# Kernel optimization log

Measured on AMD Instinct MI355X. Metric: run time of the kernel, lower is better.

Reference implementation:

```python
import jax, jax.numpy as jnp
from jax import lax
import numpy as np

# dims
B, C, H, W, T = 8, 2, 64, 64, 200
# per-layer neuron configs (defaults from NetworkBasic.__init__)
THETA = (30.0, 50.0, 100.0)
TAU_SR = (1.0, 2.0, 4.0)
TAU_REF = (1.0, 2.0, 4.0)
SCALE_REF = (1.0, 1.0, 1.0)
TAU_RHO = (1.0, 1.0, 10.0)


def psp(x, tau):
    """SLAYER synaptic response: first-order leaky integration over time axis (last).
    a[t] = exp(-1/tau) * a[t-1] + x[t]"""
    d = jnp.exp(jnp.asarray(-1.0 / tau, x.dtype))
    xt = jnp.moveaxis(x, -1, 0)  # [T, B, C, H, W]
    def step(a, xi):
        a = d * a + xi
        return a, a
    _, ys = lax.scan(step, jnp.zeros_like(xt[0]), xt)
    return jnp.moveaxis(ys, 0, -1)


def spike(u, theta, tau_ref, scale_ref, tau_rho):
    """SLAYER spiking unit: threshold + leaky refractory state, sequential over T.
    Forward emits hard spikes; surrogate (sigmoid) used only for gradients."""
    dref = jnp.exp(jnp.asarray(-1.0 / tau_ref, u.dtype))
    th = jnp.asarray(theta, u.dtype)
    ut = jnp.moveaxis(u, -1, 0)  # [T, ...]
    def step(r, ui):
        v = ui + r
        hard = (v >= th).astype(u.dtype)
        sur = jax.nn.sigmoid((v - th) / tau_rho)
        s = sur + lax.stop_gradient(hard - sur)  # straight-through surrogate
        r2 = dref * r - th * scale_ref * s       # refractory subtraction
        return r2, s
    _, s = lax.scan(step, jnp.zeros_like(ut[0]), ut)
    return jnp.moveaxis(s, 0, -1)


def conv2d_t(x, w, pad):
    """slayer.conv: spatial conv applied independently per timestep (kernel kxkx1, no bias)."""
    Bb, Cc, Hh, Ww, Tt = x.shape
    xt = jnp.moveaxis(x, -1, 1).reshape(Bb * Tt, Cc, Hh, Ww)
    y = lax.conv_general_dilated(xt, w, (1, 1), [(pad, pad), (pad, pad)],
                                 dimension_numbers=("NCHW", "OIHW", "NCHW"))
    O = w.shape[0]
    return jnp.moveaxis(y.reshape(Bb, Tt, O, Hh, Ww), 1, -1)


def convT2d_t(x, w):
    """slayer.convTranspose kernel=2 stride=2, per timestep (exact 2x upsample)."""
    Bb, Cc, Hh, Ww, Tt = x.shape
    xt = jnp.moveaxis(x, -1, 1).reshape(Bb * Tt, Cc, Hh, Ww)
    y = lax.conv_transpose(xt, w, (2, 2), "VALID",
                           dimension_numbers=("NCHW", "OIHW", "NCHW"))
    O = w.shape[0]
    return jnp.moveaxis(y.reshape(Bb, Tt, O, 2 * Hh, 2 * Ww), 1, -1)


def setup_inputs() -> dict:
    key = jax.random.key(0)
    k0, k1, k2, k3 = jax.random.split(key, 4)
    spikeInput = (jax.random.uniform(k0, (B, C, H, W, T)) < 0.3).astype(jnp.float32)
    w1 = jax.random.normal(k1, (8, 2, 5, 5), jnp.float32) * 10.0
    w2 = jax.random.normal(k2, (8, 8, 3, 3), jnp.float32) * 10.0
    wup = jax.random.normal(k3, (2, 8, 2, 2), jnp.float32) * 10.0
    return {"spikeInput": spikeInput, "w1": w1, "w2": w2, "wup": wup}


def reference(spikeInput, w1, w2, wup):
    Bb, Cc, Hh, Ww, Tt = spikeInput.shape
    psp1 = psp(spikeInput, TAU_SR[0])
    psp1_up = jax.image.resize(psp1, (Bb, Cc, 2 * Hh, 2 * Ww, Tt), method="linear")
    s1 = spike(conv2d_t(psp1, w1, 2), THETA[0], TAU_REF[0], SCALE_REF[0], TAU_RHO[0])
    s2 = spike(conv2d_t(psp(s1, TAU_SR[1]), w2, 1), THETA[1], TAU_REF[1], SCALE_REF[1], TAU_RHO[1])
    s3 = spike(convT2d_t(psp(s2, TAU_SR[2]), wup) + psp1_up,
               THETA[2], TAU_REF[2], SCALE_REF[2], TAU_RHO[2])
    return s3
```

## Files before the change

kernel.cpp:

```cpp
#include <hip/hip_runtime.h>

#define DEC1 0.36787944117144233f
#define DEC2 0.60653065971263342f
#define DEC3 0.77880078307140487f

__global__ void prep_weights(const float* __restrict__ w1,
                             const float* __restrict__ w2,
                             const float* __restrict__ wup,
                             float* __restrict__ wr)
{
    int i = blockIdx.x * 256 + threadIdx.x;
    if (i < 400) {
        int o = i & 7, tap = i >> 3;
        int c = tap / 25, rem = tap % 25, ky = rem / 5, kx = rem % 5;
        wr[i] = w1[((o * 2 + c) * 5 + ky) * 5 + kx];
    }
    if (i < 576) {
        int o = i & 7, tap = i >> 3;
        int c = tap / 9, rem = tap % 9, ky = rem / 3, kx = rem % 3;
        wr[400 + i] = w2[((o * 8 + c) * 3 + ky) * 3 + kx];
    }
    if (i < 64) {
        int c = i & 7, r = i >> 3;
        int dj = r & 1, di = (r >> 1) & 1, o = r >> 2;
        wr[976 + i] = wup[((o * 8 + c) * 2 + (1 - di)) * 2 + (1 - dj)];
    }
}

static __device__ __forceinline__ float4 spike_psp4(float4 u, float th, float dref,
                                                    float dq, float& r, float& q)
{
    float4 qv; float v, s;
    v = __fadd_rn(u.x, r); s = (v >= th) ? 1.f : 0.f;
    r = __fsub_rn(__fmul_rn(dref, r), __fmul_rn(th, s));
    q = __fadd_rn(__fmul_rn(dq, q), s); qv.x = q;
    v = __fadd_rn(u.y, r); s = (v >= th) ? 1.f : 0.f;
    r = __fsub_rn(__fmul_rn(dref, r), __fmul_rn(th, s));
    q = __fadd_rn(__fmul_rn(dq, q), s); qv.y = q;
    v = __fadd_rn(u.z, r); s = (v >= th) ? 1.f : 0.f;
    r = __fsub_rn(__fmul_rn(dref, r), __fmul_rn(th, s));
    q = __fadd_rn(__fmul_rn(dq, q), s); qv.z = q;
    v = __fadd_rn(u.w, r); s = (v >= th) ? 1.f : 0.f;
    r = __fsub_rn(__fmul_rn(dref, r), __fmul_rn(th, s));
    q = __fadd_rn(__fmul_rn(dq, q), s); qv.w = q;
    return qv;
}

static __device__ __forceinline__ float4 spike4(float4 u, float th, float dref, float& r)
{
    float4 ov; float v, s;
    v = __fadd_rn(u.x, r); s = (v >= th) ? 1.f : 0.f;
    r = __fsub_rn(__fmul_rn(dref, r), __fmul_rn(th, s)); ov.x = s;
    v = __fadd_rn(u.y, r); s = (v >= th) ? 1.f : 0.f;
    r = __fsub_rn(__fmul_rn(dref, r), __fmul_rn(th, s)); ov.y = s;
    v = __fadd_rn(u.z, r); s = (v >= th) ? 1.f : 0.f;
    r = __fsub_rn(__fmul_rn(dref, r), __fmul_rn(th, s)); ov.z = s;
    v = __fadd_rn(u.w, r); s = (v >= th) ? 1.f : 0.f;
    r = __fsub_rn(__fmul_rn(dref, r), __fmul_rn(th, s)); ov.w = s;
    return ov;
}

#define FMA4(ACC_, W_, D_) { ACC_.x += (W_)*(D_).x; ACC_.y += (W_)*(D_).y; \
                             ACC_.z += (W_)*(D_).z; ACC_.w += (W_)*(D_).w; }

#define PSP4(V_, X_, st) { \
    V_.x = __fadd_rn(__fmul_rn(DEC1, st),   X_.x); \
    V_.y = __fadd_rn(__fmul_rn(DEC1, V_.x), X_.y); \
    V_.z = __fadd_rn(__fmul_rn(DEC1, V_.y), X_.z); \
    V_.w = __fadd_rn(__fmul_rn(DEC1, V_.z), X_.w); st = V_.w; }

__global__ __launch_bounds__(256, 2)
void snn_fused(const float* __restrict__ spk,
               const float* __restrict__ wr,
               float* __restrict__ out)
{
    const int tid  = threadIdx.x;
    const int b    = blockIdx.x >> 6;
    const int tile = blockIdx.x & 63;
    const int gy0  = (tile >> 3) << 3;
    const int gx0  = (tile & 7) << 3;

    __shared__ float4 sP1[2][2][2][224];
    __shared__ float4 sP2[8][2][100];
    __shared__ float4 sP3[8][2][64];

    float aP0 = 0.f, aP1 = 0.f;
    float rB[4], qB[4];
    float rC[2] = {0.f, 0.f}, qC[2] = {0.f, 0.f};
    float r3[2] = {0.f, 0.f};
#pragma unroll
    for (int i = 0; i < 4; ++i) { rB[i] = 0.f; qB[i] = 0.f; }

    const int ary = tid / 14, arx = tid % 14;
    const int aidx = ary * 16 + arx;
    const int aiy = gy0 - 3 + ary, aix = gx0 - 3 + arx;
    const bool avalid = (tid < 196) && (aiy >= 0) && (aiy < 64) && (aix >= 0) && (aix < 64);
    const int aoff0 = avalid ? (((b * 2 + 0) * 64 + aiy) * 64 + aix) * 200 : 0;
    const int aoff1 = avalid ? (((b * 2 + 1) * 64 + aiy) * 64 + aix) * 200 : 0;

    const int ochB = __builtin_amdgcn_readfirstlane(tid >> 7);
    const int bpx  = tid & 127;
    int by_, bx_;
    if (bpx < 80) { by_ = bpx >> 3; bx_ = bpx & 7; }
    else          { int t2 = bpx - 80; by_ = t2 >> 1; bx_ = 8 + (t2 & 1); }
    const int by = by_, bx = bx_;
    const int bwr = by * 10 + bx;

    const int wvC  = __builtin_amdgcn_readfirstlane(tid >> 6);
    const int ochC = wvC * 2;
    const int cpx  = tid & 63;
    const int cy   = cpx >> 3, cx = cpx & 7;

    const int od  = tid >> 7;
    const int ddi = (tid >> 6) & 1;
    const int dpx = tid & 63;
    const int dy  = dpx >> 3, dxx = dpx & 7;
    const int diy = gy0 + dy, dix = gx0 + dxx;

    const float ay  = ddi ? ((diy == 63) ? 1.f : 0.75f) : ((diy == 0) ? 0.f : 0.25f);
    const float byw = ddi ? ((diy == 63) ? 0.f : 0.25f) : ((diy == 0) ? 1.f : 0.75f);
    const float ax0 = (dix == 0)  ? 0.f : 0.25f;
    const float bx0 = (dix == 0)  ? 1.f : 0.75f;
    const float ax1 = (dix == 63) ? 1.f : 0.75f;
    const float bx1 = (dix == 63) ? 0.f : 0.25f;
    const int   didx = (dy + 2 + ddi) * 16 + (dxx + 2);

    float4 x00 = make_float4(0.f,0.f,0.f,0.f), x01 = x00, x10 = x00, x11 = x00;
    if (avalid) {
        x00 = *(const float4*)(spk + aoff0);
        x01 = *(const float4*)(spk + aoff0 + 4);
        x10 = *(const float4*)(spk + aoff1);
        x11 = *(const float4*)(spk + aoff1 + 4);
    }

#pragma unroll 1
    for (int ck = 0; ck < 25; ++ck) {
        const int t0 = ck * 8;
        const int p  = ck & 1;

        if (tid < 196) {
            float4 v;
            PSP4(v, x00, aP0); sP1[p][0][0][aidx] = v;
            PSP4(v, x01, aP0); sP1[p][0][1][aidx] = v;
            PSP4(v, x10, aP1); sP1[p][1][0][aidx] = v;
            PSP4(v, x11, aP1); sP1[p][1][1][aidx] = v;
            if (ck < 24 && avalid) {
                x00 = *(const float4*)(spk + aoff0 + t0 + 8);
                x01 = *(const float4*)(spk + aoff0 + t0 + 12);
                x10 = *(const float4*)(spk + aoff1 + t0 + 8);
                x11 = *(const float4*)(spk + aoff1 + t0 + 12);
            }
        }
        __syncthreads();

        if (bpx < 100) {
            float4 a0[4], a1[4];
#pragma unroll
            for (int j = 0; j < 4; ++j) { a0[j] = make_float4(0.f,0.f,0.f,0.f); a1[j] = a0[j]; }
            const float* wB = wr + ochB * 4;
#pragma unroll 1
            for (int c = 0; c < 2; ++c) {
#pragma unroll 1
                for (int ky = 0; ky < 5; ++ky) {
                    const float4* r0 = &sP1[p][c][0][(by + ky) * 16 + bx];
                    const float4* r1 = &sP1[p][c][1][(by + ky) * 16 + bx];
                    const float*  wrow = wB + (c * 25 + ky * 5) * 8;
#pragma unroll
                    for (int kx = 0; kx < 5; ++kx) {
                        float4 d0 = r0[kx], d1 = r1[kx];
#pragma unroll
                        for (int j = 0; j < 4; ++j) {
                            float wv = wrow[kx * 8 + j];
                            FMA4(a0[j], wv, d0); FMA4(a1[j], wv, d1);
                        }
                    }
                }
            }
#pragma unroll
            for (int j = 0; j < 4; ++j) {
                float4 q0 = spike_psp4(a0[j], 30.f, DEC1, DEC2, rB[j], qB[j]);
                sP2[ochB * 4 + j][0][bwr] = q0;
                float4 q1 = spike_psp4(a1[j], 30.f, DEC1, DEC2, rB[j], qB[j]);
                sP2[ochB * 4 + j][1][bwr] = q1;
            }
        }
        __syncthreads();

        {
            float4 a00 = make_float4(0.f,0.f,0.f,0.f), a01 = a00, a10 = a00, a11 = a00;
            const float* wC = wr + 400 + ochC;
#pragma unroll 1
            for (int c = 0; c < 8; ++c) {
#pragma unroll 1
                for (int ky = 0; ky < 3; ++ky) {
                    const float4* r0 = &sP2[c][0][(cy + ky) * 10 + cx];
                    const float4* r1 = &sP2[c][1][(cy + ky) * 10 + cx];
                    const float*  wrow = wC + (c * 9 + ky * 3) * 8;
#pragma unroll
                    for (int kx = 0; kx < 3; ++kx) {
                        float4 d0 = r0[kx], d1 = r1[kx];
                        float w0 = wrow[kx * 8], w1 = wrow[kx * 8 + 1];
                        FMA4(a00, w0, d0); FMA4(a01, w0, d1);
                        FMA4(a10, w1, d0); FMA4(a11, w1, d1);
                    }
                }
            }
            float4 qv;
            qv = spike_psp4(a00, 50.f, DEC2, DEC3, rC[0], qC[0]); sP3[ochC][0][cpx] = qv;
            qv = spike_psp4(a01, 50.f, DEC2, DEC3, rC[0], qC[0]); sP3[ochC][1][cpx] = qv;
            qv = spike_psp4(a10, 50.f, DEC2, DEC3, rC[1], qC[1]); sP3[ochC + 1][0][cpx] = qv;
            qv = spike_psp4(a11, 50.f, DEC2, DEC3, rC[1], qC[1]); sP3[ochC + 1][1][cpx] = qv;
        }
        __syncthreads();

        {
#pragma unroll 1
            for (int h = 0; h < 2; ++h) {
                float4 p3[8];
#pragma unroll
                for (int c = 0; c < 8; ++c) p3[c] = sP3[c][h][dpx];
                float4 P0a = sP1[p][od][h][didx];
                float4 P0b = sP1[p][od][h][didx + 1];
                float4 P0c = sP1[p][od][h][didx + 2];
                float4 P1a = sP1[p][od][h][didx + 16];
                float4 P1b = sP1[p][od][h][didx + 17];
                float4 P1c = sP1[p][od][h][didx + 18];
#pragma unroll
                for (int dj = 0; dj < 2; ++dj) {
                    const float ax  = dj ? ax1 : ax0;
                    const float bxw = dj ? bx1 : bx0;
                    float4 tv = make_float4(0.f, 0.f, 0.f, 0.f);
                    const float* wD = wr + 976 + ((od * 2 + ddi) * 2 + dj) * 8;
#pragma unroll
                    for (int c = 0; c < 8; ++c) {
                        float wv = wD[c];
                        FMA4(tv, wv, p3[c]);
                    }
                    float4 A  = dj ? P0b : P0a;
                    float4 Bv = dj ? P0c : P0b;
                    float4 Cv = dj ? P1b : P1a;
                    float4 Dv = dj ? P1c : P1b;
                    float4 up, u; float ra, rb;
                    ra = __fadd_rn(__fmul_rn(ay, A.x),  __fmul_rn(byw, Cv.x));
                    rb = __fadd_rn(__fmul_rn(ay, Bv.x), __fmul_rn(byw, Dv.x));
                    up.x = __fadd_rn(__fmul_rn(ax, ra), __fmul_rn(bxw, rb));
                    ra = __fadd_rn(__fmul_rn(ay, A.y),  __fmul_rn(byw, Cv.y));
                    rb = __fadd_rn(__fmul_rn(ay, Bv.y), __fmul_rn(byw, Dv.y));
                    up.y = __fadd_rn(__fmul_rn(ax, ra), __fmul_rn(bxw, rb));
                    ra = __fadd_rn(__fmul_rn(ay, A.z),  __fmul_rn(byw, Cv.z));
                    rb = __fadd_rn(__fmul_rn(ay, Bv.z), __fmul_rn(byw, Dv.z));
                    up.z = __fadd_rn(__fmul_rn(ax, ra), __fmul_rn(bxw, rb));
                    ra = __fadd_rn(__fmul_rn(ay, A.w),  __fmul_rn(byw, Cv.w));
                    rb = __fadd_rn(__fmul_rn(ay, Bv.w), __fmul_rn(byw, Dv.w));
                    up.w = __fadd_rn(__fmul_rn(ax, ra), __fmul_rn(bxw, rb));
                    u.x = __fadd_rn(tv.x, up.x);
                    u.y = __fadd_rn(tv.y, up.y);
                    u.z = __fadd_rn(tv.z, up.z);
                    u.w = __fadd_rn(tv.w, up.w);
                    float4 ov = spike4(u, 100.f, DEC3, r3[dj]);
                    float* op = out + ((((b * 2 + od) * 128 + (2 * diy + ddi)) * 128)
                                       + (2 * dix + dj)) * 200 + t0 + h * 4;
                    *(float4*)op = ov;
                }
            }
        }
    }
}

extern "C" void kernel_launch(void* const* d_in, const int* in_sizes, int n_in,
                              void* d_out, int out_size, void* d_ws, size_t ws_size,
                              hipStream_t stream)
{
    const float* spk = (const float*)d_in[0];
    const float* w1  = (const float*)d_in[1];
    const float* w2  = (const float*)d_in[2];
    const float* wup = (const float*)d_in[3];
    float* outp = (float*)d_out;
    float* wr   = (float*)d_ws;

    prep_weights<<<dim3(3), dim3(256), 0, stream>>>(w1, w2, wup, wr);
    snn_fused<<<dim3(512), dim3(256), 0, stream>>>(spk, wr, outp);
}
```

Before: 603.8 us.

## Split conv work by time-half to reuse input loads across output channels

Conv1 and conv2 threads now compute every output channel for one time half, instead of a channel subset for both halves. Each shared-memory input float4 is then read once and reused across more output channels. Because the sequential spike/PSP recurrence needs both halves in order, raw conv outputs are written to shared memory and a second pass per layer applies the spike recurrence in place. This adds two extra __syncthreads and shared-memory round trips per chunk, and raises conv1 accumulator registers to 8 float4s.

After: 572.8 us (median of 2 runs). 5.1% less time.

```diff
diff --git a/kernel.cpp b/kernel.cpp
--- a/kernel.cpp
+++ b/kernel.cpp
@@ -98,18 +98,20 @@
     const int aoff0 = avalid ? (((b * 2 + 0) * 64 + aiy) * 64 + aix) * 200 : 0;
     const int aoff1 = avalid ? (((b * 2 + 1) * 64 + aiy) * 64 + aix) * 200 : 0;
 
-    const int ochB = __builtin_amdgcn_readfirstlane(tid >> 7);
+    const int bh   = __builtin_amdgcn_readfirstlane(tid >> 7);
     const int bpx  = tid & 127;
     int by_, bx_;
     if (bpx < 80) { by_ = bpx >> 3; bx_ = bpx & 7; }
     else          { int t2 = bpx - 80; by_ = t2 >> 1; bx_ = 8 + (t2 & 1); }
     const int by = by_, bx = bx_;
     const int bwr = by * 10 + bx;
-
-    const int wvC  = __builtin_amdgcn_readfirstlane(tid >> 6);
-    const int ochC = wvC * 2;
+    const int ochB = tid >> 7;
+
+    const int ch2  = __builtin_amdgcn_readfirstlane(tid >> 7);
+    const int cop  = __builtin_amdgcn_readfirstlane(tid >> 6) & 1;
     const int cpx  = tid & 63;
     const int cy   = cpx >> 3, cx = cpx & 7;
+    const int och2 = (tid >> 6) * 2;
 
     const int od  = tid >> 7;
     const int ddi = (tid >> 6) & 1;
@@ -154,62 +156,83 @@
         __syncthreads();
 
         if (bpx < 100) {
-            float4 a0[4], a1[4];
-#pragma unroll
-            for (int j = 0; j < 4; ++j) { a0[j] = make_float4(0.f,0.f,0.f,0.f); a1[j] = a0[j]; }
-            const float* wB = wr + ochB * 4;
+            float4 a[8];
+#pragma unroll
+            for (int o = 0; o < 8; ++o) a[o] = make_float4(0.f,0.f,0.f,0.f);
 #pragma unroll 1
             for (int c = 0; c < 2; ++c) {
 #pragma unroll 1
                 for (int ky = 0; ky < 5; ++ky) {
-                    const float4* r0 = &sP1[p][c][0][(by + ky) * 16 + bx];
-                    const float4* r1 = &sP1[p][c][1][(by + ky) * 16 + bx];
-                    const float*  wrow = wB + (c * 25 + ky * 5) * 8;
+                    const float4* r0 = &sP1[p][c][bh][(by + ky) * 16 + bx];
+                    const float*  wrow = wr + (c * 25 + ky * 5) * 8;
 #pragma unroll
                     for (int kx = 0; kx < 5; ++kx) {
-                        float4 d0 = r0[kx], d1 = r1[kx];
-#pragma unroll
-                        for (int j = 0; j < 4; ++j) {
-                            float wv = wrow[kx * 8 + j];
-                            FMA4(a0[j], wv, d0); FMA4(a1[j], wv, d1);
+                        float4 d = r0[kx];
+#pragma unroll
+                        for (int o = 0; o < 8; ++o) {
+                            float wv = wrow[kx * 8 + o];
+                            FMA4(a[o], wv, d);
                         }
                     }
                 }
             }
 #pragma unroll
+            for (int o = 0; o < 8; ++o) sP2[o][bh][bwr] = a[o];
+        }
+        __syncthreads();
+
+        if (bpx < 100) {
+#pragma unroll
             for (int j = 0; j < 4; ++j) {
-                float4 q0 = spike_psp4(a0[j], 30.f, DEC1, DEC2, rB[j], qB[j]);
-                sP2[ochB * 4 + j][0][bwr] = q0;
-                float4 q1 = spike_psp4(a1[j], 30.f, DEC1, DEC2, rB[j], qB[j]);
-                sP2[ochB * 4 + j][1][bwr] = q1;
+                const int o = ochB * 4 + j;
+                float4 u0 = sP2[o][0][bwr];
+                float4 u1 = sP2[o][1][bwr];
+                float4 q0 = spike_psp4(u0, 30.f, DEC1, DEC2, rB[j], qB[j]);
+                sP2[o][0][bwr] = q0;
+                float4 q1 = spike_psp4(u1, 30.f, DEC1, DEC2, rB[j], qB[j]);
+                sP2[o][1][bwr] = q1;
             }
         }
         __syncthreads();
 
         {
-            float4 a00 = make_float4(0.f,0.f,0.f,0.f), a01 = a00, a10 = a00, a11 = a00;
-            const float* wC = wr + 400 + ochC;
+            float4 a[4];
+#pragma unroll
+            for (int j = 0; j < 4; ++j) a[j] = make_float4(0.f,0.f,0.f,0.f);
+            const float* wC = wr + 400 + cop * 4;
 #pragma unroll 1
             for (int c = 0; c < 8; ++c) {
 #pragma unroll 1
                 for (int ky = 0; ky < 3; ++ky) {
-                    const float4* r0 = &sP2[c][0][(cy + ky) * 10 + cx];
-                    const float4* r1 = &sP2[c][1][(cy + ky) * 10 + cx];
+                    const float4* r0 = &sP2[c][ch2][(cy + ky) * 10 + cx];
                     const float*  wrow = wC + (c * 9 + ky * 3) * 8;
 #pragma unroll
                     for (int kx = 0; kx < 3; ++kx) {
-                        float4 d0 = r0[kx], d1 = r1[kx];
-                        float w0 = wrow[kx * 8], w1 = wrow[kx * 8 + 1];
-                        FMA4(a00, w0, d0); FMA4(a01, w0, d1);
-                        FMA4(a10, w1, d0); FMA4(a11, w1, d1);
+                        float4 d = r0[kx];
+#pragma unroll
+                        for (int j = 0; j < 4; ++j) {
+                            float wv = wrow[kx * 8 + j];
+                            FMA4(a[j], wv, d);
+                        }
                     }
                 }
             }
-            float4 qv;
-            qv = spike_psp4(a00, 50.f, DEC2, DEC3, rC[0], qC[0]); sP3[ochC][0][cpx] = qv;
-            qv = spike_psp4(a01, 50.f, DEC2, DEC3, rC[0], qC[0]); sP3[ochC][1][cpx] = qv;
-            qv = spike_psp4(a10, 50.f, DEC2, DEC3, rC[1], qC[1]); sP3[ochC + 1][0][cpx] = qv;
-            qv = spike_psp4(a11, 50.f, DEC2, DEC3, rC[1], qC[1]); sP3[ochC + 1][1][cpx] = qv;
+#pragma unroll
+            for (int j = 0; j < 4; ++j) sP3[cop * 4 + j][ch2][cpx] = a[j];
+        }
+        __syncthreads();
+
+        {
+#pragma unroll
+            for (int j = 0; j < 2; ++j) {
+                const int o = och2 + j;
+                float4 u0 = sP3[o][0][cpx];
+                float4 u1 = sP3[o][1][cpx];
+                float4 q0 = spike_psp4(u0, 50.f, DEC2, DEC3, rC[j], qC[j]);
+                sP3[o][0][cpx] = q0;
+                float4 q1 = spike_psp4(u1, 50.f, DEC2, DEC3, rC[j], qC[j]);
+                sP3[o][1][cpx] = q1;
+            }
         }
         __syncthreads();
 
```
